# Kernel optimization log

Measured on AMD Instinct MI355X. Metric: run time of the kernel, lower is better.

Reference implementation:

```python
import jax, jax.numpy as jnp
import numpy as np

DIM = 2048
NH = 16
NKV = 4
HD = DIM // NH            # 128
KVD = HD * NKV            # 512
MLP = int(DIM * 4.0 * 2 / 3)  # 5461
EPS = 1.1920929e-07       # torch.finfo(float32).eps (nn.RMSNorm default)
ROPE_BASE = 10000.0


def act_quant(x):
    # per-token int8 absmax quantization (BitNet b1.58)
    scale = 127.0 / jnp.clip(jnp.max(jnp.abs(x), axis=-1, keepdims=True), 1e-5)
    return jnp.clip(jnp.round(x * scale), -128.0, 127.0) / scale


def weight_quant(w):
    # ternary weights via mean-absmax scale (BitNet b1.58)
    scale = 1.0 / jnp.clip(jnp.mean(jnp.abs(w)), 1e-5)
    return jnp.clip(jnp.round(w * scale), -1.0, 1.0) / scale


def bitlinear(x, w, b=None):
    # straight-through estimator quantization, then dense matmul
    xq = x + jax.lax.stop_gradient(act_quant(x) - x)
    wq = w + jax.lax.stop_gradient(weight_quant(w) - w)
    y = xq @ wq.T
    return y if b is None else y + b


def rmsnorm(x, w):
    return x * jax.lax.rsqrt(jnp.mean(x * x, axis=-1, keepdims=True) + EPS) * w


def rope_cos_sin(pos, head_dim, dtype):
    inv_freq = 1.0 / (ROPE_BASE ** (jnp.arange(0, head_dim, 2, dtype=jnp.float32) / head_dim))
    freqs = pos[..., None].astype(jnp.float32) * inv_freq  # [B,N,HD/2]
    cos = jnp.repeat(jnp.cos(freqs), 2, axis=-1).astype(dtype)  # interleaved [B,N,HD]
    sin = jnp.repeat(jnp.sin(freqs), 2, axis=-1).astype(dtype)
    return cos, sin


def rotate_interleave(x):
    x1 = x[..., 0::2]
    x2 = x[..., 1::2]
    return jnp.stack([-x2, x1], axis=-1).reshape(x.shape)


def apply_rope(x, cos, sin):
    # x: [B,H,N,HD]; cos/sin: [B,N,HD]
    return x * cos[:, None] + rotate_interleave(x) * sin[:, None]


def setup_inputs() -> dict:
    key = jax.random.key(0)
    ks = jax.random.split(key, 16)
    B, N = 2, 2048
    s = 0.02
    return {
        "x": jax.random.normal(ks[0], (B, N, DIM), jnp.float32),
        "position_ids": jnp.broadcast_to(jnp.arange(N, dtype=jnp.int32), (B, N)),
        "norm1_w": jnp.ones((DIM,), jnp.float32),
        "q_w": jax.random.normal(ks[1], (DIM, DIM), jnp.float32) * s,
        "q_b": jnp.zeros((DIM,), jnp.float32),
        "k_w": jax.random.normal(ks[2], (KVD, DIM), jnp.float32) * s,
        "k_b": jnp.zeros((KVD,), jnp.float32),
        "v_w": jax.random.normal(ks[3], (KVD, DIM), jnp.float32) * s,
        "v_b": jnp.zeros((KVD,), jnp.float32),
        "o_w": jax.random.normal(ks[4], (DIM, DIM), jnp.float32) * s,
        "norm2_w": jnp.ones((DIM,), jnp.float32),
        "gate_w": jax.random.normal(ks[5], (MLP, DIM), jnp.float32) * s,
        "up_w": jax.random.normal(ks[6], (MLP, DIM), jnp.float32) * s,
        "down_w": jax.random.normal(ks[7], (DIM, MLP), jnp.float32) * s,
    }


def reference(x, position_ids, norm1_w, q_w, q_b, k_w, k_b, v_w, v_b, o_w,
              norm2_w, gate_w, up_w, down_w):
    B, N, C = x.shape
    # --- attention ---
    h = rmsnorm(x, norm1_w)
    q = bitlinear(h, q_w, q_b).reshape(B, N, NH, HD).transpose(0, 2, 1, 3)
    k = bitlinear(h, k_w, k_b).reshape(B, N, NKV, HD).transpose(0, 2, 1, 3)
    v = bitlinear(h, v_w, v_b).reshape(B, N, NKV, HD).transpose(0, 2, 1, 3)
    cos, sin = rope_cos_sin(position_ids, HD, x.dtype)
    q = apply_rope(q, cos, sin)
    k = apply_rope(k, cos, sin)
    g = NH // NKV
    k = jnp.repeat(k, g, axis=1)  # GQA head expansion -> [B,NH,N,HD]
    v = jnp.repeat(v, g, axis=1)
    scores = jnp.einsum('bhqd,bhkd->bhqk', q, k) * (HD ** -0.5)
    causal_mask = jnp.triu(jnp.ones((N, N), bool), 1)
    scores = jnp.where(causal_mask, -jnp.inf, scores)
    attn = jax.nn.softmax(scores, axis=-1)
    out = jnp.einsum('bhqk,bhkd->bqhd', attn, v).reshape(B, N, C)
    x = x + bitlinear(out, o_w)
    # --- SwiGLU MLP ---
    h = rmsnorm(x, norm2_w)
    x = x + bitlinear(jax.nn.silu(bitlinear(h, gate_w)) * bitlinear(h, up_w), down_w)
    return x
```

## Files before the change

### kernel.cpp

```cpp
#include <hip/hip_runtime.h>

typedef unsigned short u16;
typedef unsigned int   u32;
typedef unsigned char  u8;

using bf16x8 = __attribute__((ext_vector_type(8))) short;
using f32x4  = __attribute__((ext_vector_type(4))) float;
using i32x4  = __attribute__((ext_vector_type(4))) int;

#define SEQ    2048
#define DIMC   2048
#define TOK    4096
#define QKV_N  3072
#define GU_N   11008
#define MLP_P  5504
#define MLP_R  5461
#define ATT_SCALE 0.08838834764831845f

__device__ __forceinline__ float bf2f(u16 v){ return __uint_as_float(((u32)v) << 16); }
__device__ __forceinline__ u16 f2bf(float f){
  u32 x = __float_as_uint(f);
  u32 r = (x + 0x7fffu + ((x >> 16) & 1u)) >> 16;
  return (u16)r;
}

__device__ __forceinline__ float waveRedSum(float v){
#pragma unroll
  for (int o = 32; o > 0; o >>= 1) v += __shfl_xor(v, o);
  return v;
}
__device__ __forceinline__ float waveRedMax(float v){
#pragma unroll
  for (int o = 32; o > 0; o >>= 1) v = fmaxf(v, __shfl_xor(v, o));
  return v;
}

#define GLD16(gp, lp) __builtin_amdgcn_global_load_lds( \
    (__attribute__((address_space(1))) void*)(gp), \
    (__attribute__((address_space(3))) void*)(lp), 16, 0, 0)

#define FENCE() asm volatile("" ::: "memory")
#define SBAR()  do{ FENCE(); __builtin_amdgcn_s_barrier(); FENCE(); }while(0)
#define VMCNT(n) asm volatile("s_waitcnt vmcnt(" #n ")" ::: "memory")

__global__ __launch_bounds__(256) void k_abssum7(
    const float4* __restrict__ w0, const float4* __restrict__ w1,
    const float4* __restrict__ w2, const float4* __restrict__ w3,
    const float4* __restrict__ w4, const float4* __restrict__ w5,
    const float4* __restrict__ w6, float* __restrict__ sc){
  const int rg = blockIdx.y;
  const float4* w = rg==0?w0: rg==1?w1: rg==2?w2: rg==3?w3: rg==4?w4: rg==5?w5: w6;
  const int n4 = (rg==0||rg==3) ? 1048576 : (rg<4 ? 262144 : 2796032);
  float s = 0.f;
  for (int i = blockIdx.x*256 + threadIdx.x; i < n4; i += gridDim.x*256){
    float4 v = w[i];
    s += fabsf(v.x) + fabsf(v.y) + fabsf(v.z) + fabsf(v.w);
  }
  s = waveRedSum(s);
  __shared__ float sm[4];
  int lane = threadIdx.x & 63, wv = threadIdx.x >> 6;
  if (lane == 0) sm[wv] = s;
  __syncthreads();
  if (threadIdx.x == 0) atomicAdd(sc + rg, sm[0]+sm[1]+sm[2]+sm[3]);
}

__global__ void k_finalize(float* __restrict__ sc){
  if (threadIdx.x == 0){
    const float counts[7] = {4194304.f, 1048576.f, 1048576.f, 4194304.f,
                             11184128.f, 11184128.f, 11184128.f};
    for (int i = 0; i < 7; i++) sc[8+i] = fmaxf(sc[i]/counts[i], 1e-5f);
  }
}

__global__ __launch_bounds__(256) void k_wquant6(
    const float4* __restrict__ w0, const float4* __restrict__ w1,
    const float4* __restrict__ w2, const float4* __restrict__ w3,
    const float4* __restrict__ w4, const float4* __restrict__ w5,
    u32* __restrict__ d0, u32* __restrict__ d1, u32* __restrict__ d2,
    u32* __restrict__ d3, u32* __restrict__ d4, u32* __restrict__ d5,
    const float* __restrict__ sc){
  const int rg = blockIdx.y;
  const float4* src = rg==0?w0: rg==1?w1: rg==2?w2: rg==3?w3: rg==4?w4: w5;
  u32* dst = rg==0?d0: rg==1?d1: rg==2?d2: rg==3?d3: rg==4?d4: d5;
  const int n4 = (rg==0||rg==3) ? 1048576 : (rg<4 ? 262144 : 2796032);
  float ws = 1.0f / sc[8+rg];
  for (int i = blockIdx.x*256 + threadIdx.x; i < n4; i += gridDim.x*256){
    float4 v = src[i];
    int c0 = (int)fminf(fmaxf(rintf(v.x*ws), -1.f), 1.f);
    int c1 = (int)fminf(fmaxf(rintf(v.y*ws), -1.f), 1.f);
    int c2 = (int)fminf(fmaxf(rintf(v.z*ws), -1.f), 1.f);
    int c3 = (int)fminf(fmaxf(rintf(v.w*ws), -1.f), 1.f);
    dst[i] = (u32)(u8)c0 | ((u32)(u8)c1 << 8) | ((u32)(u8)c2 << 16) | ((u32)(u8)c3 << 24);
  }
}

__global__ __launch_bounds__(256) void k_wquant_down(const float* __restrict__ src,
                                                     u32* __restrict__ dst,
                                                     const float* __restrict__ deqp){
  int i = blockIdx.x*256 + threadIdx.x;
  const int total = 2048*(MLP_P/4);
  if (i >= total) return;
  float ws = 1.0f / deqp[0];
  int r = i / (MLP_P/4);
  int c4 = (i - r*(MLP_P/4))*4;
  u32 o = 0;
#pragma unroll
  for (int e = 0; e < 4; e++){
    int c = c4 + e;
    int t = 0;
    if (c < MLP_R) t = (int)fminf(fmaxf(rintf(src[(long)r*MLP_R + c]*ws), -1.f), 1.f);
    o |= (u32)(u8)t << (8*e);
  }
  dst[i] = o;
}

__global__ __launch_bounds__(256) void k_rmsq(const float* __restrict__ in,
                                              const float* __restrict__ nw,
                                              char* __restrict__ outq,
                                              float* __restrict__ rowdeq, int do_norm){
  const int row = blockIdx.x, tid = threadIdx.x;
  const float* xp = in + (long)row * DIMC + tid*8;
  float v[8];
  float4 a0 = *(const float4*)xp;
  float4 a1 = *(const float4*)(xp + 4);
  v[0]=a0.x; v[1]=a0.y; v[2]=a0.z; v[3]=a0.w;
  v[4]=a1.x; v[5]=a1.y; v[6]=a1.z; v[7]=a1.w;
  float ss = 0.f;
#pragma unroll
  for (int j = 0; j < 8; j++) ss += v[j]*v[j];
  __shared__ float sm[8];
  int lane = tid & 63, wv = tid >> 6;
  ss = waveRedSum(ss);
  if (lane == 0) sm[wv] = ss;
  __syncthreads();
  float h[8];
  float amax = 0.f;
  if (do_norm){
    float tot = sm[0]+sm[1]+sm[2]+sm[3];
    float rms = rsqrtf(tot * (1.0f/DIMC) + 1.1920929e-07f);
    float4 w0 = *(const float4*)(nw + tid*8);
    float4 w1 = *(const float4*)(nw + tid*8 + 4);
    float wr8[8] = {w0.x,w0.y,w0.z,w0.w,w1.x,w1.y,w1.z,w1.w};
#pragma unroll
    for (int j = 0; j < 8; j++){ h[j] = v[j]*rms*wr8[j]; amax = fmaxf(amax, fabsf(h[j])); }
  } else {
#pragma unroll
    for (int j = 0; j < 8; j++){ h[j] = v[j]; amax = fmaxf(amax, fabsf(h[j])); }
  }
  amax = waveRedMax(amax);
  if (lane == 0) sm[4+wv] = amax;
  __syncthreads();
  float gmax = fmaxf(fmaxf(sm[4],sm[5]), fmaxf(sm[6],sm[7]));
  float sc = 127.0f / fmaxf(gmax, 1e-5f);
  int2 o;
  char* oc = (char*)&o;
#pragma unroll
  for (int j = 0; j < 8; j++)
    oc[j] = (char)(int)fminf(fmaxf(rintf(h[j]*sc), -128.f), 127.f);
  *(int2*)(outq + (long)row*DIMC + tid*8) = o;
  if (tid == 0) rowdeq[row] = 1.0f / sc;
}

__global__ __launch_bounds__(256) void k_ropevt(u16* __restrict__ y,
                                                const int* __restrict__ pos_ids,
                                                u16* __restrict__ VT){
  if (blockIdx.x < 20480){
    int idx = blockIdx.x*256 + threadIdx.x;
    int m = idx / 1280;
    int p = idx - m*1280;
    int c = p*2;
    int i = (c & 127) >> 1;
    float pos = (float)pos_ids[m];
    float inv = expf((float)i * -0.14391156831212787f);
    float f = pos * inv;
    float sn, cs;
    sincosf(f, &sn, &cs);
    u32* pr = (u32*)(y + (long)m*QKV_N + c);
    u32 both = *pr;
    float x0 = bf2f((u16)(both & 0xffffu));
    float x1 = bf2f((u16)(both >> 16));
    u16 o0 = f2bf(x0*cs - x1*sn);
    u16 o1 = f2bf(x1*cs + x0*sn);
    *pr = (u32)o0 | ((u32)o1 << 16);
  } else {
    int idx = (blockIdx.x - 20480)*256 + threadIdx.x;
    int d  = idx & 127;
    int hk = (idx >> 7) & 3;
    int b  = (idx >> 9) & 1;
    int tg = idx >> 10;
    int tok0 = tg*8;
    const u16* src = y + ((long)b*SEQ + tok0)*QKV_N + 2560 + hk*128 + d;
    u16 tmp[8];
#pragma unroll
    for (int e = 0; e < 8; e++) tmp[e] = src[(long)e*QKV_N];
    *(int4*)(VT + (((long)(b*4+hk))*128 + d)*SEQ + tok0) = *(int4*)tmp;
  }
}

template<int BM, int BN, int WM, int WN, int MODE>
__global__ __launch_bounds__(512, 2) void k_gemm8(
    const char* __restrict__ A, const char* __restrict__ B,
    int K, int lda, int ldb, int ldc, int ntn,
    const float* __restrict__ rowdeq, const float* __restrict__ deqp,
    const float* __restrict__ bq, const float* __restrict__ bk, const float* __restrict__ bv,
    const float* __restrict__ resid, float* __restrict__ outF, u16* __restrict__ outB)
{
  constexpr int SM = BM/WM, SN = BN/WN;
  constexpr int MR = SM/16, NR = SN/16, MRH = MR/2;
  constexpr int RA = BM/128, RB = BN/128;
  constexpr int ASZ = BM*64, BSZ = BN*64;
  constexpr int BUFSZ = 2*(ASZ+BSZ);
  extern __shared__ __align__(16) char sm8[];

  const int tid = threadIdx.x;
  const int lane = tid & 63, wv = tid >> 6;
  const int wr = wv / WN, wc = wv % WN;
  const int r = lane & 15, qq = lane >> 4;

  const int nwg = gridDim.x;
  const int chunk = nwg >> 3;
  const int lin = blockIdx.x;
  const int swz = (lin & 7)*chunk + (lin >> 3);
  const int mt = swz / ntn, nt = swz - mt*ntn;
  const long m0 = (long)mt*BM, n0 = (long)nt*BN;

  const char* __restrict__ gA = A + m0*lda;
  const char* __restrict__ gB = B + n0*ldb;

  int  soA[RA], soB[RB];
  long goA[RA], goB[RB];
#pragma unroll
  for (int u = 0; u < RA; u++){
    int c = u*512 + tid, row = c >> 2, gp = c & 3, g = gp ^ ((row>>1)&3);
    soA[u] = c*16; goA[u] = (long)row*lda + g*16;
  }
#pragma unroll
  for (int u = 0; u < RB; u++){
    int c = u*512 + tid, row = c >> 2, gp = c & 3, g = gp ^ ((row>>1)&3);
    soB[u] = c*16; goB[u] = (long)row*ldb + g*16;
  }
  const int gsw = (qq ^ ((r>>1)&3))*16;
  const int aoff0 = (wr*SM + r)*64 + gsw;
  const int boff0 = (wc*SN + r)*64 + gsw;

  const int NT = K >> 7;

  i32x4 acc[MR][NR];
#pragma unroll
  for (int i = 0; i < MR; i++)
#pragma unroll
    for (int j = 0; j < NR; j++) acc[i][j] = (i32x4){0,0,0,0};

  auto stA = [&](int tq, int kh){
    char* dst = sm8 + (tq&1)*BUFSZ + kh*ASZ;
    const char* src = gA + (long)tq*128 + kh*64;
#pragma unroll
    for (int u = 0; u < RA; u++) GLD16(src + goA[u], dst + soA[u]);
  };
  auto stB = [&](int tq, int kh){
    char* dst = sm8 + (tq&1)*BUFSZ + 2*ASZ + kh*BSZ;
    const char* src = gB + (long)tq*128 + kh*64;
#pragma unroll
    for (int u = 0; u < RB; u++) GLD16(src + goB[u], dst + soB[u]);
  };

  stA(0,0); stB(0,0); stA(0,1); stB(0,1);
  stA(1,0); stB(1,0);
  if constexpr (RA+RB == 4) VMCNT(4); else VMCNT(3);
  SBAR();

  for (int t = 0; t < NT; t++){
    const char* cA = sm8 + (t&1)*BUFSZ;
    const char* cB = cA + 2*ASZ;
    i32x4 bF[NR];
    {
      i32x4 aF[MRH];
#pragma unroll
      for (int i = 0; i < MRH; i++) aF[i] = *(const i32x4*)(cA + aoff0 + i*1024);
#pragma unroll
      for (int j = 0; j < NR; j++)  bF[j] = *(const i32x4*)(cB + boff0 + j*1024);
      if (t+1 < NT) stA(t+1, 1);
      SBAR();
      __builtin_amdgcn_s_setprio(1);
#pragma unroll
      for (int i = 0; i < MRH; i++)
#pragma unroll
        for (int j = 0; j < NR; j++)
          acc[i][j] = __builtin_amdgcn_mfma_i32_16x16x64_i8(aF[i], bF[j], acc[i][j], 0,0,0);
      __builtin_amdgcn_s_setprio(0);
      SBAR();
    }
    {
      i32x4 aF[MRH];
#pragma unroll
      for (int i = 0; i < MRH; i++) aF[i] = *(const i32x4*)(cA + aoff0 + (MRH+i)*1024);
      if (t+1 < NT) stB(t+1, 1);
      SBAR();
      __builtin_amdgcn_s_setprio(1);
#pragma unroll
      for (int i = 0; i < MRH; i++)
#pragma unroll
        for (int j = 0; j < NR; j++)
          acc[MRH+i][j] = __builtin_amdgcn_mfma_i32_16x16x64_i8(aF[i], bF[j], acc[MRH+i][j], 0,0,0);
      __builtin_amdgcn_s_setprio(0);
      SBAR();
    }
    {
      i32x4 aF[MRH];
#pragma unroll
      for (int i = 0; i < MRH; i++) aF[i] = *(const i32x4*)(cA + ASZ + aoff0 + i*1024);
#pragma unroll
      for (int j = 0; j < NR; j++)  bF[j] = *(const i32x4*)(cB + BSZ + boff0 + j*1024);
      if (t+2 < NT) stA(t+2, 0);
      SBAR();
      __builtin_amdgcn_s_setprio(1);
#pragma unroll
      for (int i = 0; i < MRH; i++)
#pragma unroll
        for (int j = 0; j < NR; j++)
          acc[i][j] = __builtin_amdgcn_mfma_i32_16x16x64_i8(aF[i], bF[j], acc[i][j], 0,0,0);
      __builtin_amdgcn_s_setprio(0);
      SBAR();
    }
    {
      i32x4 aF[MRH];
#pragma unroll
      for (int i = 0; i < MRH; i++) aF[i] = *(const i32x4*)(cA + ASZ + aoff0 + (MRH+i)*1024);
      if (t+2 < NT) stB(t+2, 0);
      SBAR();
      __builtin_amdgcn_s_setprio(1);
#pragma unroll
      for (int i = 0; i < MRH; i++)
#pragma unroll
        for (int j = 0; j < NR; j++)
          acc[MRH+i][j] = __builtin_amdgcn_mfma_i32_16x16x64_i8(aF[i], bF[j], acc[MRH+i][j], 0,0,0);
      __builtin_amdgcn_s_setprio(0);
      if (t + 1 < NT){
        if (t + 2 < NT){ if constexpr (RA+RB == 4) VMCNT(4); else VMCNT(3); }
        else VMCNT(0);
      }
      SBAR();
    }
  }

#pragma unroll
  for (int i = 0; i < MR; i++){
#pragma unroll
    for (int tt = 0; tt < 4; tt++){
      const long row = m0 + wr*SM + 16*i + 4*qq + tt;
      const float rdv = rowdeq[row];
#pragma unroll
      for (int j = 0; j < NR; j++){
        const long col = n0 + wc*SN + 16*j + r;
        float vv = (float)acc[i][j][tt];
        if constexpr (MODE == 0){
          int sec = (col >= 2048) + (col >= 2560);
          float dq = deqp[sec];
          float bias = (sec == 0) ? bq[col] : (sec == 1) ? bk[col-2048] : bv[col-2560];
          outB[row*(long)ldc + col] = f2bf(vv*rdv*dq + bias);
        } else if constexpr (MODE == 1){
          outF[row*(long)ldc + col] = vv*rdv*deqp[0] + resid[row*(long)ldc + col];
        } else {
          int sec = (col >= 5504) ? 1 : 0;
          outB[row*(long)ldc + col] = f2bf(vv*rdv*deqp[sec]);
        }
      }
    }
  }
}

__global__ __launch_bounds__(256) void k_attn(const u16* __restrict__ Y,
                                              const u16* __restrict__ VT,
                                              float* __restrict__ O)
{
  __shared__ u16 Ks[64*128];
  __shared__ u16 VTs[128*64];
  __shared__ u16 Ps[64][72];

  const int pp = blockIdx.x;
  const int bh = blockIdx.y;
  const int b = bh >> 4, h = bh & 15, hk = h >> 2;
  const int tid = threadIdx.x;
  const int lane = tid & 63, wv = tid >> 6;
  const int r = lane & 15, qq = lane >> 4;
  const long rowbase = (long)b * SEQ;
  const u16* Kbase = Y + rowbase*QKV_N + 2048 + hk*128;
  const u16* Vbase = VT + ((long)(b*4+hk))*128*SEQ;

  for (int ph = 0; ph < 2; ph++){
    const int qt = ph ? pp : 31 - pp;
    const int q0 = qt * 64;

    bf16x8 qf[4];
#pragma unroll
    for (int kc = 0; kc < 4; kc++)
      qf[kc] = *(const bf16x8*)(Y + (rowbase + q0 + wv*16 + r)*QKV_N + h*128 + kc*32 + qq*8);

#pragma unroll
    for (int rnd = 0; rnd < 4; rnd++){
      int c = rnd*256 + tid;
      int row = c >> 4, g = (c & 15) ^ (row & 7);
      GLD16(Kbase + ((long)(qt*0 + row))*QKV_N + g*8, (char*)Ks + c*16);
    }
#pragma unroll
    for (int rnd = 0; rnd < 4; rnd++){
      int c = rnd*256 + tid;
      int d = c >> 3, g = (c & 7) ^ (d & 7);
      GLD16(Vbase + (long)d*SEQ + g*8, (char*)VTs + c*16);
    }
    __syncthreads();

    f32x4 accO[8];
#pragma unroll
    for (int jn = 0; jn < 8; jn++) accO[jn] = (f32x4){0.f,0.f,0.f,0.f};
    float m_run[4] = {-INFINITY,-INFINITY,-INFINITY,-INFINITY};
    float l_run[4] = {0.f,0.f,0.f,0.f};

    for (int kt = 0; kt <= qt; kt++){
      float sv[4][4];
#pragma unroll
      for (int j = 0; j < 4; j++){
        f32x4 a = (f32x4){0.f,0.f,0.f,0.f};
#pragma unroll
        for (int kc = 0; kc < 4; kc++){
          bf16x8 kf = *(const bf16x8*)(Ks + (16*j + r)*128 + (((kc*4 + qq) ^ (r & 7)))*8);
          a = __builtin_amdgcn_mfma_f32_16x16x32_bf16(qf[kc], kf, a, 0, 0, 0);
        }
#pragma unroll
        for (int t = 0; t < 4; t++) sv[j][t] = a[t] * ATT_SCALE;
      }
      __syncthreads();
      if (kt < qt){
#pragma unroll
        for (int rnd = 0; rnd < 4; rnd++){
          int c = rnd*256 + tid;
          int row = c >> 4, g = (c & 15) ^ (row & 7);
          GLD16(Kbase + ((long)((kt+1)*64 + row))*QKV_N + g*8, (char*)Ks + c*16);
        }
      }
      if (kt == qt){
#pragma unroll
        for (int j = 0; j < 4; j++){
          int key = kt*64 + 16*j + r;
#pragma unroll
          for (int t = 0; t < 4; t++){
            int qr = q0 + wv*16 + 4*qq + t;
            if (key > qr) sv[j][t] = -INFINITY;
          }
        }
      }
#pragma unroll
      for (int t = 0; t < 4; t++){
        float mm = fmaxf(fmaxf(sv[0][t],sv[1][t]), fmaxf(sv[2][t],sv[3][t]));
#pragma unroll
        for (int o = 8; o > 0; o >>= 1) mm = fmaxf(mm, __shfl_xor(mm, o));
        float mnew = fmaxf(m_run[t], mm);
        float alpha = __expf(m_run[t] - mnew);
        m_run[t] = mnew;
        float ps = 0.f;
#pragma unroll
        for (int j = 0; j < 4; j++){
          float p = __expf(sv[j][t] - mnew);
          ps += p;
          Ps[wv*16 + 4*qq + t][16*j + r] = f2bf(p);
        }
#pragma unroll
        for (int o = 8; o > 0; o >>= 1) ps += __shfl_xor(ps, o);
        l_run[t] = l_run[t]*alpha + ps;
#pragma unroll
        for (int jn = 0; jn < 8; jn++) accO[jn][t] *= alpha;
      }
#pragma unroll
      for (int kc = 0; kc < 2; kc++){
        bf16x8 pf = *(const bf16x8*)&Ps[wv*16 + r][kc*32 + qq*8];
#pragma unroll
        for (int jn = 0; jn < 8; jn++){
          bf16x8 vf = *(const bf16x8*)(VTs + (16*jn + r)*64 + (((kc*4 + qq) ^ (r & 7)))*8);
          accO[jn] = __builtin_amdgcn_mfma_f32_16x16x32_bf16(pf, vf, accO[jn], 0, 0, 0);
        }
      }
      __syncthreads();
      if (kt < qt){
#pragma unroll
        for (int rnd = 0; rnd < 4; rnd++){
          int c = rnd*256 + tid;
          int d = c >> 3, g = (c & 7) ^ (d & 7);
          GLD16(Vbase + (long)d*SEQ + (kt+1)*64 + g*8, (char*)VTs + c*16);
        }
      }
    }
    float inv[4];
#pragma unroll
    for (int t = 0; t < 4; t++) inv[t] = 1.0f / l_run[t];
#pragma unroll
    for (int jn = 0; jn < 8; jn++){
#pragma unroll
      for (int t = 0; t < 4; t++){
        long row = rowbase + q0 + wv*16 + 4*qq + t;
        O[row*DIMC + h*128 + 16*jn + r] = accO[jn][t]*inv[t];
      }
    }
    __syncthreads();
  }
}

__global__ __launch_bounds__(256) void k_swiglu(const u16* __restrict__ ygu,
                                                char* __restrict__ qout,
                                                float* __restrict__ rowdeq){
  const int row = blockIdx.x, tid = threadIdx.x;
  const u16* base = ygu + (long)row * GU_N;
  float h[24];
  float amax = 0.f;
#pragma unroll
  for (int it = 0; it < 3; it++){
    int chunk = it*256 + tid;
    if (chunk < 688){
      int j0 = chunk*8;
      int4 g4 = *(const int4*)(base + j0);
      int4 u4 = *(const int4*)(base + MLP_P + j0);
      const u16* gp = (const u16*)&g4;
      const u16* up = (const u16*)&u4;
#pragma unroll
      for (int e = 0; e < 8; e++){
        float g = bf2f(gp[e]);
        float u = bf2f(up[e]);
        float hv = g * (1.0f/(1.0f + __expf(-g))) * u;
        h[it*8+e] = hv;
        amax = fmaxf(amax, fabsf(hv));
      }
    } else {
#pragma unroll
      for (int e = 0; e < 8; e++) h[it*8+e] = 0.f;
    }
  }
  amax = waveRedMax(amax);
  __shared__ float sm[4];
  int lane = tid & 63, wv = tid >> 6;
  if (lane == 0) sm[wv] = amax;
  __syncthreads();
  float gmax = fmaxf(fmaxf(sm[0],sm[1]), fmaxf(sm[2],sm[3]));
  float sc = 127.0f / fmaxf(gmax, 1e-5f);
#pragma unroll
  for (int it = 0; it < 3; it++){
    int chunk = it*256 + tid;
    if (chunk < 688){
      int j0 = chunk*8;
      int2 o;
      char* oc = (char*)&o;
#pragma unroll
      for (int e = 0; e < 8; e++)
        oc[e] = (char)(int)fminf(fmaxf(rintf(h[it*8+e]*sc), -128.f), 127.f);
      *(int2*)(qout + (long)row*MLP_P + j0) = o;
    }
  }
  if (tid == 0) rowdeq[row] = 1.0f/sc;
}

extern "C" void kernel_launch(void* const* d_in, const int* in_sizes, int n_in,
                              void* d_out, int out_size, void* d_ws, size_t ws_size,
                              hipStream_t stream)
{
  (void)in_sizes; (void)n_in; (void)out_size; (void)ws_size;
  const float* x   = (const float*)d_in[0];
  const int*   pos = (const int*)d_in[1];
  const float* n1w = (const float*)d_in[2];
  const float* qw  = (const float*)d_in[3];
  const float* qb  = (const float*)d_in[4];
  const float* kw  = (const float*)d_in[5];
  const float* kb  = (const float*)d_in[6];
  const float* vw  = (const float*)d_in[7];
  const float* vb  = (const float*)d_in[8];
  const float* ow  = (const float*)d_in[9];
  const float* n2w = (const float*)d_in[10];
  const float* gw  = (const float*)d_in[11];
  const float* uw  = (const float*)d_in[12];
  const float* dw  = (const float*)d_in[13];
  float* out = (float*)d_out;
  char* ws = (char*)d_ws;

  static int attr_done = 0;
  if (!attr_done){
    hipFuncSetAttribute(reinterpret_cast<const void*>(k_gemm8<256,128,4,2,0>),
                        hipFuncAttributeMaxDynamicSharedMemorySize, 98304);
    hipFuncSetAttribute(reinterpret_cast<const void*>(k_gemm8<256,128,4,2,1>),
                        hipFuncAttributeMaxDynamicSharedMemorySize, 98304);
    hipFuncSetAttribute(reinterpret_cast<const void*>(k_gemm8<256,256,2,4,2>),
                        hipFuncAttributeMaxDynamicSharedMemorySize, 131072);
    attr_done = 1;
  }

  float* sc   = (float*)ws;
  char* Wqkv  = ws + 256;
  char* Wo    = ws + 6291712;
  char* Wgu   = ws + 10486016;
  char* Wd    = ws + 33030400;
  char* actq  = ws + 44302592;
  char* swq   = ws + 52691200;
  float* rd   = (float*)(ws + 75235584);
  char* xreg  = ws + 75252224;
  u16* yqkv   = (u16*)xreg;
  float* attn = (float*)(xreg + 25165824);
  u16* vT     = (u16*)(xreg + 58720256);
  u16* ygu    = (u16*)xreg;

  hipMemsetAsync(sc, 0, 64, stream);
  k_abssum7<<<dim3(512,7),256,0,stream>>>((const float4*)qw, (const float4*)kw,
                                          (const float4*)vw, (const float4*)ow,
                                          (const float4*)gw, (const float4*)uw,
                                          (const float4*)dw, sc);
  k_finalize<<<1,64,0,stream>>>(sc);
  k_wquant6<<<dim3(512,6),256,0,stream>>>((const float4*)qw, (const float4*)kw,
                                          (const float4*)vw, (const float4*)ow,
                                          (const float4*)gw, (const float4*)uw,
                                          (u32*)Wqkv, (u32*)(Wqkv + 2048l*2048),
                                          (u32*)(Wqkv + 2560l*2048), (u32*)Wo,
                                          (u32*)Wgu, (u32*)(Wgu + 5504l*2048), sc);
  hipMemsetAsync(Wgu + 5461l*2048,        0, 43l*2048, stream);
  hipMemsetAsync(Wgu + (5504l+5461)*2048, 0, 43l*2048, stream);
  k_wquant_down<<<11008,256,0,stream>>>(dw, (u32*)Wd, sc+14);

  k_rmsq<<<4096,256,0,stream>>>(x, n1w, actq, rd, 1);
  k_gemm8<256,128,4,2,0><<<384,512,98304,stream>>>(actq, Wqkv, 2048, 2048, 2048, 3072, 24,
                                          rd, sc+8, qb, kb, vb, nullptr, nullptr, yqkv);
  k_ropevt<<<21504,256,0,stream>>>(yqkv, pos, vT);
  k_attn<<<dim3(16,32),256,0,stream>>>(yqkv, vT, attn);
  k_rmsq<<<4096,256,0,stream>>>(attn, n1w, actq, rd, 0);
  k_gemm8<256,128,4,2,1><<<256,512,98304,stream>>>(actq, Wo, 2048, 2048, 2048, 2048, 16,
                                          rd, sc+11, nullptr, nullptr, nullptr, x, out, nullptr);

  k_rmsq<<<4096,256,0,stream>>>(out, n2w, actq, rd, 1);
  k_gemm8<256,256,2,4,2><<<688,512,131072,stream>>>(actq, Wgu, 2048, 2048, 2048, 11008, 43,
                                          rd, sc+12, nullptr, nullptr, nullptr, nullptr, nullptr, ygu);
  k_swiglu<<<4096,256,0,stream>>>(ygu, swq, rd);
  k_gemm8<256,128,4,2,1><<<256,512,98304,stream>>>(swq, Wd, 5504, 5504, 5504, 2048, 16,
                                          rd, sc+14, nullptr, nullptr, nullptr, out, out, nullptr);
}
```

Baseline: 684.3 us.

## Replace templated int8 GEMM with 4-wave 256x128 kernel using 64-wide K steps

Replaces the templated 8-wave int8 MFMA GEMM with a fixed 4-wave kernel (256 threads). Each wave computes a 128x64 sub-tile of a 256x128 block tile. The K step drops from 128 to 64, and the double buffer now uses 48KB of static LDS instead of up to 128KB of dynamic LDS. The gate/up GEMM moves from 256x256 to 256x128 tiles, which doubles its grid. The prefetch schedule is reworked so A is loaded one step ahead and B two steps ahead. The intent is higher occupancy and fewer barriers per MFMA, at the cost of less data reuse per block and more per-wave register pressure.

```diff
diff --git a/kernel.cpp b/kernel.cpp
--- a/kernel.cpp
+++ b/kernel.cpp
@@ -197,24 +197,24 @@
   }
 }
 
-template<int BM, int BN, int WM, int WN, int MODE>
-__global__ __launch_bounds__(512, 2) void k_gemm8(
+template<int MODE>
+__global__ __launch_bounds__(256, 2) void k_gemm2b(
     const char* __restrict__ A, const char* __restrict__ B,
     int K, int lda, int ldb, int ldc, int ntn,
     const float* __restrict__ rowdeq, const float* __restrict__ deqp,
     const float* __restrict__ bq, const float* __restrict__ bk, const float* __restrict__ bv,
     const float* __restrict__ resid, float* __restrict__ outF, u16* __restrict__ outB)
 {
-  constexpr int SM = BM/WM, SN = BN/WN;
-  constexpr int MR = SM/16, NR = SN/16, MRH = MR/2;
-  constexpr int RA = BM/128, RB = BN/128;
+  constexpr int BM = 256, BN = 128;
+  constexpr int MR = 8, NR = 4, MRH = 4;
+  constexpr int RA = 4, RB = 2;
   constexpr int ASZ = BM*64, BSZ = BN*64;
-  constexpr int BUFSZ = 2*(ASZ+BSZ);
-  extern __shared__ __align__(16) char sm8[];
+  constexpr int BUFSZ = ASZ + BSZ;
+  __shared__ __align__(16) char sm8[2*BUFSZ];
 
   const int tid = threadIdx.x;
   const int lane = tid & 63, wv = tid >> 6;
-  const int wr = wv / WN, wc = wv % WN;
+  const int wr = wv >> 1, wc = wv & 1;
   const int r = lane & 15, qq = lane >> 4;
 
   const int nwg = gridDim.x;
@@ -231,19 +231,19 @@
   long goA[RA], goB[RB];
 #pragma unroll
   for (int u = 0; u < RA; u++){
-    int c = u*512 + tid, row = c >> 2, gp = c & 3, g = gp ^ ((row>>1)&3);
+    int c = u*256 + tid, row = c >> 2, g = (c & 3) ^ ((row>>1)&3);
     soA[u] = c*16; goA[u] = (long)row*lda + g*16;
   }
 #pragma unroll
   for (int u = 0; u < RB; u++){
-    int c = u*512 + tid, row = c >> 2, gp = c & 3, g = gp ^ ((row>>1)&3);
+    int c = u*256 + tid, row = c >> 2, g = (c & 3) ^ ((row>>1)&3);
     soB[u] = c*16; goB[u] = (long)row*ldb + g*16;
   }
   const int gsw = (qq ^ ((r>>1)&3))*16;
-  const int aoff0 = (wr*SM + r)*64 + gsw;
-  const int boff0 = (wc*SN + r)*64 + gsw;
-
-  const int NT = K >> 7;
+  const int aoff0 = (wr*128 + r)*64 + gsw;
+  const int boff0 = (wc*64 + r)*64 + gsw;
+
+  const int NT = K >> 6;
 
   i32x4 acc[MR][NR];
 #pragma unroll
@@ -251,27 +251,26 @@
 #pragma unroll
     for (int j = 0; j < NR; j++) acc[i][j] = (i32x4){0,0,0,0};
 
-  auto stA = [&](int tq, int kh){
-    char* dst = sm8 + (tq&1)*BUFSZ + kh*ASZ;
-    const char* src = gA + (long)tq*128 + kh*64;
+  auto stA = [&](int tq){
+    char* dst = sm8 + (tq&1)*BUFSZ;
+    const char* src = gA + (long)tq*64;
 #pragma unroll
     for (int u = 0; u < RA; u++) GLD16(src + goA[u], dst + soA[u]);
   };
-  auto stB = [&](int tq, int kh){
-    char* dst = sm8 + (tq&1)*BUFSZ + 2*ASZ + kh*BSZ;
-    const char* src = gB + (long)tq*128 + kh*64;
+  auto stB = [&](int tq){
+    char* dst = sm8 + (tq&1)*BUFSZ + ASZ;
+    const char* src = gB + (long)tq*64;
 #pragma unroll
     for (int u = 0; u < RB; u++) GLD16(src + goB[u], dst + soB[u]);
   };
 
-  stA(0,0); stB(0,0); stA(0,1); stB(0,1);
-  stA(1,0); stB(1,0);
-  if constexpr (RA+RB == 4) VMCNT(4); else VMCNT(3);
+  stA(0); stB(0); stB(1);
+  VMCNT(2);
   SBAR();
 
   for (int t = 0; t < NT; t++){
     const char* cA = sm8 + (t&1)*BUFSZ;
-    const char* cB = cA + 2*ASZ;
+    const char* cB = cA + ASZ;
     i32x4 bF[NR];
     {
       i32x4 aF[MRH];
@@ -279,7 +278,7 @@
       for (int i = 0; i < MRH; i++) aF[i] = *(const i32x4*)(cA + aoff0 + i*1024);
 #pragma unroll
       for (int j = 0; j < NR; j++)  bF[j] = *(const i32x4*)(cB + boff0 + j*1024);
-      if (t+1 < NT) stA(t+1, 1);
+      if (t+1 < NT) stA(t+1);
       SBAR();
       __builtin_amdgcn_s_setprio(1);
 #pragma unroll
@@ -294,39 +293,7 @@
       i32x4 aF[MRH];
 #pragma unroll
       for (int i = 0; i < MRH; i++) aF[i] = *(const i32x4*)(cA + aoff0 + (MRH+i)*1024);
-      if (t+1 < NT) stB(t+1, 1);
-      SBAR();
-      __builtin_amdgcn_s_setprio(1);
-#pragma unroll
-      for (int i = 0; i < MRH; i++)
-#pragma unroll
-        for (int j = 0; j < NR; j++)
-          acc[MRH+i][j] = __builtin_amdgcn_mfma_i32_16x16x64_i8(aF[i], bF[j], acc[MRH+i][j], 0,0,0);
-      __builtin_amdgcn_s_setprio(0);
-      SBAR();
-    }
-    {
-      i32x4 aF[MRH];
-#pragma unroll
-      for (int i = 0; i < MRH; i++) aF[i] = *(const i32x4*)(cA + ASZ + aoff0 + i*1024);
-#pragma unroll
-      for (int j = 0; j < NR; j++)  bF[j] = *(const i32x4*)(cB + BSZ + boff0 + j*1024);
-      if (t+2 < NT) stA(t+2, 0);
-      SBAR();
-      __builtin_amdgcn_s_setprio(1);
-#pragma unroll
-      for (int i = 0; i < MRH; i++)
-#pragma unroll
-        for (int j = 0; j < NR; j++)
-          acc[i][j] = __builtin_amdgcn_mfma_i32_16x16x64_i8(aF[i], bF[j], acc[i][j], 0,0,0);
-      __builtin_amdgcn_s_setprio(0);
-      SBAR();
-    }
-    {
-      i32x4 aF[MRH];
-#pragma unroll
-      for (int i = 0; i < MRH; i++) aF[i] = *(const i32x4*)(cA + ASZ + aoff0 + (MRH+i)*1024);
-      if (t+2 < NT) stB(t+2, 0);
+      if (t+2 < NT) stB(t+2);
       SBAR();
       __builtin_amdgcn_s_setprio(1);
 #pragma unroll
@@ -336,8 +303,7 @@
           acc[MRH+i][j] = __builtin_amdgcn_mfma_i32_16x16x64_i8(aF[i], bF[j], acc[MRH+i][j], 0,0,0);
       __builtin_amdgcn_s_setprio(0);
       if (t + 1 < NT){
-        if (t + 2 < NT){ if constexpr (RA+RB == 4) VMCNT(4); else VMCNT(3); }
-        else VMCNT(0);
+        if (t + 2 < NT) VMCNT(2); else VMCNT(0);
       }
       SBAR();
     }
@@ -347,11 +313,11 @@
   for (int i = 0; i < MR; i++){
 #pragma unroll
     for (int tt = 0; tt < 4; tt++){
-      const long row = m0 + wr*SM + 16*i + 4*qq + tt;
+      const long row = m0 + wr*128 + 16*i + 4*qq + tt;
       const float rdv = rowdeq[row];
 #pragma unroll
       for (int j = 0; j < NR; j++){
-        const long col = n0 + wc*SN + 16*j + r;
+        const long col = n0 + wc*64 + 16*j + r;
         float vv = (float)acc[i][j][tt];
         if constexpr (MODE == 0){
           int sec = (col >= 2048) + (col >= 2560);
@@ -578,17 +544,6 @@
   float* out = (float*)d_out;
   char* ws = (char*)d_ws;
 
-  static int attr_done = 0;
-  if (!attr_done){
-    hipFuncSetAttribute(reinterpret_cast<const void*>(k_gemm8<256,128,4,2,0>),
-                        hipFuncAttributeMaxDynamicSharedMemorySize, 98304);
-    hipFuncSetAttribute(reinterpret_cast<const void*>(k_gemm8<256,128,4,2,1>),
-                        hipFuncAttributeMaxDynamicSharedMemorySize, 98304);
-    hipFuncSetAttribute(reinterpret_cast<const void*>(k_gemm8<256,256,2,4,2>),
-                        hipFuncAttributeMaxDynamicSharedMemorySize, 131072);
-    attr_done = 1;
-  }
-
   float* sc   = (float*)ws;
   char* Wqkv  = ws + 256;
   char* Wo    = ws + 6291712;
@@ -620,18 +575,18 @@
   k_wquant_down<<<11008,256,0,stream>>>(dw, (u32*)Wd, sc+14);
 
   k_rmsq<<<4096,256,0,stream>>>(x, n1w, actq, rd, 1);
-  k_gemm8<256,128,4,2,0><<<384,512,98304,stream>>>(actq, Wqkv, 2048, 2048, 2048, 3072, 24,
-                                          rd, sc+8, qb, kb, vb, nullptr, nullptr, yqkv);
+  k_gemm2b<0><<<384,256,0,stream>>>(actq, Wqkv, 2048, 2048, 2048, 3072, 24,
+                                    rd, sc+8, qb, kb, vb, nullptr, nullptr, yqkv);
   k_ropevt<<<21504,256,0,stream>>>(yqkv, pos, vT);
   k_attn<<<dim3(16,32),256,0,stream>>>(yqkv, vT, attn);
   k_rmsq<<<4096,256,0,stream>>>(attn, n1w, actq, rd, 0);
-  k_gemm8<256,128,4,2,1><<<256,512,98304,stream>>>(actq, Wo, 2048, 2048, 2048, 2048, 16,
-                                          rd, sc+11, nullptr, nullptr, nullptr, x, out, nullptr);
+  k_gemm2b<1><<<256,256,0,stream>>>(actq, Wo, 2048, 2048, 2048, 2048, 16,
+                                    rd, sc+11, nullptr, nullptr, nullptr, x, out, nullptr);
 
   k_rmsq<<<4096,256,0,stream>>>(out, n2w, actq, rd, 1);
-  k_gemm8<256,256,2,4,2><<<688,512,131072,stream>>>(actq, Wgu, 2048, 2048, 2048, 11008, 43,
-                                          rd, sc+12, nullptr, nullptr, nullptr, nullptr, nullptr, ygu);
+  k_gemm2b<2><<<1376,256,0,stream>>>(actq, Wgu, 2048, 2048, 2048, 11008, 86,
+                                     rd, sc+12, nullptr, nullptr, nullptr, nullptr, nullptr, ygu);
   k_swiglu<<<4096,256,0,stream>>>(ygu, swq, rd);
-  k_gemm8<256,128,4,2,1><<<256,512,98304,stream>>>(swq, Wd, 5504, 5504, 5504, 2048, 16,
-                                          rd, sc+14, nullptr, nullptr, nullptr, out, out, nullptr);
-}
+  k_gemm2b<1><<<256,256,0,stream>>>(swq, Wd, 5504, 5504, 5504, 2048, 16,
+                                    rd, sc+14, nullptr, nullptr, nullptr, out, out, nullptr);
+}
```

New measurement: 694.5 us. No clear change (+1.5%).
